# Optimization experiments

Hardware: AMD Instinct MI355X
Metric: run time of the kernel (lower is better)

## Reference

```python
import jax, jax.numpy as jnp
import numpy as np

NUM_HEADS = 8
TOPK = 16


def setup_inputs() -> dict:
    key = jax.random.key(0)
    ks = jax.random.split(key, 13)
    B, C, H, W = 2, 512, 64, 64
    Hu, Wu = H // 2, W // 2
    hd = C // NUM_HEADS
    n = lambda k, shape, s=1.0: jax.random.normal(k, shape, dtype=jnp.float32) * s
    return {
        "x": n(ks[0], (B, C, H, W)),
        "upper_feat": n(ks[1], (B, C, Hu, Wu)),
        "gumbel": jax.random.gumbel(ks[2], (B, NUM_HEADS, Hu * Wu), dtype=jnp.float32),
        # 1x1 convs (Conv2d + folded eval-mode BN => weight matrix + bias)
        "q_w": n(ks[3], (C, C), 0.02), "q_b": n(ks[4], (C,), 0.02),
        "kv_w": n(ks[5], (2 * C, C), 0.02), "kv_b": n(ks[6], (2 * C,), 0.02),
        "proj_w": n(ks[7], (C, C), 0.02), "proj_b": n(ks[8], (C,), 0.02),
        # depthwise 7x7 PE conv (groups = C)
        "pe_w": n(ks[9], (C, 1, 7, 7), 0.02), "pe_b": n(ks[10], (C,), 0.02),
        # gate conv1d kernel_size=1: [head_dim, 2*head_dim]
        "gate_w": n(ks[11], (hd, 2 * hd), 0.02), "gate_b": n(ks[12], (hd,), 0.02),
    }


def reference(x, upper_feat, gumbel, q_w, q_b, kv_w, kv_b, proj_w, proj_b,
              pe_w, pe_b, gate_w, gate_b):
    B, C, H, W = x.shape
    hd = C // NUM_HEADS
    Hu, Wu = upper_feat.shape[2], upper_feat.shape[3]
    N, Nu = H * W, Hu * Wu
    scale = hd ** -0.5

    def conv1x1(t, w, b):
        return jnp.einsum('bchw,oc->bohw', t, w) + b[None, :, None, None]

    # coarse attention: q from x, k/v from upper_feat
    q = conv1x1(x, q_w, q_b).reshape(B, NUM_HEADS, hd, N).transpose(0, 1, 3, 2)          # [B,h,N,d]
    kv = conv1x1(upper_feat, kv_w, kv_b).reshape(B, NUM_HEADS, 2 * hd, Nu).transpose(0, 1, 3, 2)
    k, v = kv[..., :hd], kv[..., hd:]                                                    # [B,h,Nu,d]
    sim = jnp.einsum('bhnd,bhmd->bhnm', q, k) * scale                                    # [B,h,N,Nu]
    attn = jax.nn.softmax(sim, axis=-1)
    coarse = jnp.einsum('bhnm,bhmd->bhnd', attn, v)                                      # [B,h,N,d]

    # fine branch: kv from x, top-k token selection via gumbel-softmax scores
    f_kv = conv1x1(x, kv_w, kv_b).reshape(B, NUM_HEADS, 2 * hd, N).transpose(0, 1, 3, 2)
    f_k, f_v = f_kv[..., :hd], f_kv[..., hd:]                                            # [B,h,N,d]

    # heat: channel-mean of x, adaptive-avg-pooled 2x2 to upper resolution (no grad)
    heat = jax.lax.stop_gradient(
        x.mean(axis=1).reshape(B, Hu, 2, Wu, 2).mean(axis=(2, 4)).reshape(B, Nu))
    global_sim = sim.mean(axis=2) * heat[:, None, :]                                     # [B,h,Nu]
    soft_weights = jax.nn.softmax(global_sim + gumbel, axis=-1)
    _, idx = jax.lax.top_k(soft_weights, TOPK)                                           # [B,h,K]

    # map each selected upper-token to its 2x2 block of x-tokens
    h_idx = (idx // Wu) * 2
    w_idx = (idx % Wu) * 2
    idx_full = jnp.concatenate(
        [(h_idx + dh) * W + (w_idx + dw) for dh in range(2) for dw in range(2)], axis=-1)  # [B,h,4K]

    topk_k = jnp.take_along_axis(f_k, idx_full[..., None], axis=2)                       # [B,h,4K,d]
    topk_v = jnp.take_along_axis(f_v, idx_full[..., None], axis=2)
    fine = jax.nn.softmax(jnp.einsum('bhnd,bhmd->bhnm', q, topk_k) * scale, axis=-1)
    refined = jnp.einsum('bhnm,bhmd->bhnd', fine, topk_v)                                # [B,h,N,d]

    # gated fusion (conv1d kernel_size=1 == per-token linear over 2d channels)
    fusion = jnp.concatenate([coarse, refined], axis=-1)                                 # [B,h,N,2d]
    gate = jax.nn.sigmoid(jnp.einsum('bhnc,oc->bhno', fusion, gate_w) + gate_b)
    out = gate * refined + (1.0 - gate) * coarse                                         # [B,h,N,d]

    x_out = out.transpose(0, 1, 3, 2).reshape(B, C, H, W)

    # positional encoding: depthwise 7x7 conv on v, bilinear upsample to (H,W)
    v_rs = v.transpose(0, 1, 3, 2).reshape(B, C, Hu, Wu)
    v_pe = jax.lax.conv_general_dilated(
        v_rs, pe_w, (1, 1), ((3, 3), (3, 3)), feature_group_count=C,
        dimension_numbers=('NCHW', 'OIHW', 'NCHW')) + pe_b[None, :, None, None]
    v_pe = jax.image.resize(v_pe, (B, C, H, W), method='bilinear')

    return conv1x1(x_out + v_pe, proj_w, proj_b)
```

## Files before the change

kernel.cpp:

```cpp
#include <hip/hip_runtime.h>
#include <hip/hip_bf16.h>
#include <cstdint>

typedef __hip_bfloat16 bf16;
typedef unsigned short u16;
typedef __attribute__((ext_vector_type(8))) short bf16x8;
typedef __attribute__((ext_vector_type(4))) float f32x4;

static __device__ __forceinline__ float b2f(bf16 v) { return __bfloat162float(v); }
static __device__ __forceinline__ float bs2f(u16 s) {
  unsigned int u = ((unsigned int)s) << 16;
  float f;
  __builtin_memcpy(&f, &u, 4);
  return f;
}
static __device__ __forceinline__ u16 f2bs(float f) {
  bf16 h = __float2bfloat16(f);
  u16 s;
  __builtin_memcpy(&s, &h, 2);
  return s;
}
static __device__ __forceinline__ float ldf(const void* p, size_t i, int f32) {
  return f32 ? ((const float*)p)[i] : bs2f(((const u16*)p)[i]);
}

__global__ __launch_bounds__(256) void detect_dtype(const uint4* __restrict__ xs,
                                                    int* __restrict__ flag) {
  int i = blockIdx.x * 256 + threadIdx.x;
  uint4 v = xs[i];
  bool hit = false;
#pragma unroll
  for (int j = 0; j < 4; ++j) {
    unsigned w = (j == 0) ? v.x : (j == 1) ? v.y : (j == 2) ? v.z : v.w;
    if ((w & 0x7F80u) == 0x7F80u) hit = true;
    if ((w & 0x7F800000u) == 0x7F800000u) hit = true;
  }
  unsigned long long mask = __ballot(hit);
  if (mask != 0ull && (threadIdx.x & 63) == 0) atomicOr(flag, 1);
}

__global__ __launch_bounds__(256) void prep_gate(
    const void* __restrict__ gate_w, const void* __restrict__ gate_b,
    u16* __restrict__ gwb, float* __restrict__ gbf,
    const int* __restrict__ dtf) {
  const int f32 = *dtf;
  int t = threadIdx.x;
  for (int i = t; i < 8192; i += 256)
    gwb[i] = f32 ? f2bs(((const float*)gate_w)[i]) : ((const u16*)gate_w)[i];
  if (t < 64) gbf[t] = ldf(gate_b, t, f32);
}

__global__ __launch_bounds__(256) void transpose_bf16(
    const void* __restrict__ src, u16* __restrict__ dst, int N,
    const int* __restrict__ dtf) {
  const int f32 = *dtf;
  const int b = blockIdx.z, n0 = blockIdx.x * 64, c0 = blockIdx.y * 64;
  const int t = threadIdx.x;
  __shared__ __align__(16) u16 tile[64][72];
#pragma unroll
  for (int j = 0; j < 2; ++j) {
    int cc = (t >> 3) + j * 32;
    int nn = (t & 7) * 8;
    u16 tmp[8];
    if (f32) {
      const float* s4 = (const float*)src + ((size_t)(b * 512 + c0 + cc)) * N + n0 + nn;
#pragma unroll
      for (int u = 0; u < 8; ++u) tmp[u] = f2bs(s4[u]);
    } else {
      *reinterpret_cast<uint4*>(tmp) = *reinterpret_cast<const uint4*>(
          (const u16*)src + ((size_t)(b * 512 + c0 + cc)) * N + n0 + nn);
    }
    *reinterpret_cast<uint4*>(&tile[cc][nn]) = *reinterpret_cast<const uint4*>(tmp);
  }
  __syncthreads();
#pragma unroll
  for (int j = 0; j < 2; ++j) {
    int nn = (t >> 3) + j * 32;
    int cc0 = (t & 7) * 8;
    u16 tmp[8];
#pragma unroll
    for (int u = 0; u < 8; ++u) tmp[u] = tile[cc0 + u][nn];
    *reinterpret_cast<uint4*>(&dst[((size_t)b * N + n0 + nn) * 512 + c0 + cc0]) =
        *reinterpret_cast<const uint4*>(tmp);
  }
}

template<int MODE>
__global__ __launch_bounds__(256) void gemm_mfma(
    const u16* __restrict__ A, const void* __restrict__ W,
    const void* __restrict__ bias, u16* __restrict__ o0, u16* __restrict__ o1,
    u16* __restrict__ oT, void* __restrict__ ob, int M,
    const int* __restrict__ dtf) {
  const int f32 = *dtf;
  const int b = blockIdx.z, m0 = blockIdx.x * 64, oo0 = blockIdx.y * 64;
  const int t = threadIdx.x, w = t >> 6, lane = t & 63;
  const int quad = lane >> 4, c = lane & 15;
  __shared__ __align__(16) u16 As[64][72];
  __shared__ __align__(16) u16 Ws[64][72];
  f32x4 acc[4];
#pragma unroll
  for (int ot = 0; ot < 4; ++ot) acc[ot] = (f32x4){0.f, 0.f, 0.f, 0.f};
  const u16* Ab = A + (size_t)b * M * 512;
  const int srow = t >> 2, scol = (t & 3) * 16;

  for (int k0 = 0; k0 < 512; k0 += 64) {
    __syncthreads();
    {
      const u16* ga = Ab + (size_t)(m0 + srow) * 512 + k0 + scol;
      *reinterpret_cast<uint4*>(&As[srow][scol])     = *reinterpret_cast<const uint4*>(ga);
      *reinterpret_cast<uint4*>(&As[srow][scol + 8]) = *reinterpret_cast<const uint4*>(ga + 8);
      if (f32) {
        const float* gw = (const float*)W + (size_t)(oo0 + srow) * 512 + k0 + scol;
#pragma unroll
        for (int e = 0; e < 16; ++e) Ws[srow][scol + e] = f2bs(gw[e]);
      } else {
        const u16* gw = (const u16*)W + (size_t)(oo0 + srow) * 512 + k0 + scol;
        *reinterpret_cast<uint4*>(&Ws[srow][scol])     = *reinterpret_cast<const uint4*>(gw);
        *reinterpret_cast<uint4*>(&Ws[srow][scol + 8]) = *reinterpret_cast<const uint4*>(gw + 8);
      }
    }
    __syncthreads();
#pragma unroll
    for (int ks = 0; ks < 2; ++ks) {
      bf16x8 av = *reinterpret_cast<const bf16x8*>(&As[w * 16 + c][ks * 32 + quad * 8]);
#pragma unroll
      for (int ot = 0; ot < 4; ++ot) {
        bf16x8 wv = *reinterpret_cast<const bf16x8*>(&Ws[ot * 16 + c][ks * 32 + quad * 8]);
        if (MODE == 3)
          acc[ot] = __builtin_amdgcn_mfma_f32_16x16x32_bf16(wv, av, acc[ot], 0, 0, 0);
        else
          acc[ot] = __builtin_amdgcn_mfma_f32_16x16x32_bf16(av, wv, acc[ot], 0, 0, 0);
      }
    }
  }

  if (MODE == 0) {
#pragma unroll
    for (int ot = 0; ot < 4; ++ot) {
      int o = oo0 + ot * 16 + c;
      float bv = ldf(bias, o, f32);
      int h = o >> 6, d = o & 63;
#pragma unroll
      for (int r = 0; r < 4; ++r) {
        int m = m0 + w * 16 + quad * 4 + r;
        o0[((size_t)(b * 8 + h) * M + m) * 64 + d] = f2bs(acc[ot][r] + bv);
      }
    }
  } else if (MODE == 1) {
#pragma unroll
    for (int ot = 0; ot < 4; ++ot) {
      int o = oo0 + ot * 16 + c;
      float bv = ldf(bias, o, f32);
      int hh = o >> 7, jj = o & 127;
#pragma unroll
      for (int r = 0; r < 4; ++r) {
        int m = m0 + w * 16 + quad * 4 + r;
        u16 val = f2bs(acc[ot][r] + bv);
        if (jj < 64) {
          o0[((size_t)(b * 8 + hh) * M + m) * 64 + jj] = val;
        } else {
          o1[((size_t)(b * 8 + hh) * M + m) * 64 + (jj & 63)] = val;
          oT[((size_t)(b * 8 + hh) * 64 + (jj & 63)) * M + m] = val;
        }
      }
    }
  } else {
#pragma unroll
    for (int ot = 0; ot < 4; ++ot) {
#pragma unroll
      for (int r = 0; r < 4; ++r) {
        int o = oo0 + ot * 16 + quad * 4 + r;
        float val = acc[ot][r] + ldf(bias, o, f32);
        int m = m0 + w * 16 + c;
        size_t oi_ = ((size_t)(b * 512 + o)) * M + m;
        if (f32) ((float*)ob)[oi_] = val;
        else     ((u16*)ob)[oi_] = f2bs(val);
      }
    }
  }
}

__global__ __launch_bounds__(256) void heat_kernel(const u16* __restrict__ xT,
                                                   float* __restrict__ heat) {
  int bm = blockIdx.x;
  int b = bm >> 10, mu = bm & 1023;
  int hu = mu >> 5, wu = mu & 31;
  int t = threadIdx.x;
  int row = t >> 6, seg = t & 63;
  int y = hu * 2 + (row >> 1), xx = wu * 2 + (row & 1);
  const uint4* p = reinterpret_cast<const uint4*>(
      xT + ((size_t)b * 4096 + y * 64 + xx) * 512);
  uint4 v = p[seg];
  float s = 0.f;
#pragma unroll
  for (int j = 0; j < 4; ++j) {
    unsigned w = (j == 0) ? v.x : (j == 1) ? v.y : (j == 2) ? v.z : v.w;
    s += bs2f((u16)(w & 0xFFFF)) + bs2f((u16)(w >> 16));
  }
  __shared__ float r[256];
  r[t] = s; __syncthreads();
  for (int off = 128; off; off >>= 1) { if (t < off) r[t] += r[t + off]; __syncthreads(); }
  if (t == 0) heat[bm] = r[0] * (1.0f / 2048.0f);
}

__global__ __launch_bounds__(256) void qsum_partial(const u16* __restrict__ q,
                                                    float* __restrict__ qsumP) {
  int bh = blockIdx.x, ch = blockIdx.y, t = threadIdx.x;
  int d = t & 63, g = t >> 6;
  int n0 = ch * 256 + g * 64;
  float s = 0.f;
  for (int r = 0; r < 64; ++r)
    s += bs2f(q[((size_t)bh * 4096 + n0 + r) * 64 + d]);
  __shared__ float r[256];
  r[t] = s; __syncthreads();
  if (t < 64) qsumP[(size_t)(bh * 16 + ch) * 64 + t] = r[t] + r[t + 64] + r[t + 128] + r[t + 192];
}

__global__ __launch_bounds__(256) void topk_kernel(
    const float* __restrict__ qsumP, const u16* __restrict__ k,
    const float* __restrict__ heat, const void* __restrict__ gumbel,
    int* __restrict__ posb, const int* __restrict__ dtf) {
  const int f32 = *dtf;
  int bh = blockIdx.x, b = bh >> 3, t = threadIdx.x;
  __shared__ float qs[64];
  __shared__ float s[1024];
  __shared__ float rv[256];
  __shared__ int   ri[256];
  if (t < 64) {
    float acc = 0.f;
    for (int ch = 0; ch < 16; ++ch) acc += qsumP[(size_t)(bh * 16 + ch) * 64 + t];
    qs[t] = acc;
  }
  __syncthreads();
  for (int j = 0; j < 4; ++j) {
    int m = t + j * 256;
    const u16* kr = k + ((size_t)bh * 1024 + m) * 64;
    float dot = 0.f;
    for (int d = 0; d < 64; ++d) dot += qs[d] * bs2f(kr[d]);
    s[m] = dot * (0.125f / 4096.0f) * heat[b * 1024 + m] + ldf(gumbel, (size_t)bh * 1024 + m, f32);
  }
  __syncthreads();
  for (int it = 0; it < 16; ++it) {
    float bv = -1e30f; int bi = 0x7fffffff;
    for (int j = 0; j < 4; ++j) {
      int m = t + j * 256; float vv = s[m];
      if (vv > bv || (vv == bv && m < bi)) { bv = vv; bi = m; }
    }
    rv[t] = bv; ri[t] = bi; __syncthreads();
    for (int off = 128; off; off >>= 1) {
      if (t < off) {
        if (rv[t + off] > rv[t] || (rv[t + off] == rv[t] && ri[t + off] < ri[t])) {
          rv[t] = rv[t + off]; ri[t] = ri[t + off];
        }
      }
      __syncthreads();
    }
    if (t == 0) {
      int mi = ri[0]; s[mi] = -1e30f;
      int hy = (mi >> 5) * 2, wx = (mi & 31) * 2;
      posb[bh * 64 + it]      = hy * 64 + wx;
      posb[bh * 64 + 16 + it] = hy * 64 + wx + 1;
      posb[bh * 64 + 32 + it] = (hy + 1) * 64 + wx;
      posb[bh * 64 + 48 + it] = (hy + 1) * 64 + wx + 1;
    }
    __syncthreads();
  }
}

__global__ __launch_bounds__(256) void gather_kv_mfma(
    const u16* __restrict__ xT, const void* __restrict__ kv_w,
    const void* __restrict__ kv_b, const int* __restrict__ posb,
    u16* __restrict__ tkb, u16* __restrict__ tvTb,
    const int* __restrict__ dtf) {
  const int f32 = *dtf;
  const int bh = blockIdx.x, b = bh >> 3, h = bh & 7;
  const int half = blockIdx.y;
  const int t = threadIdx.x, w = t >> 6, lane = t & 63;
  const int quad = lane >> 4, c = lane & 15;
  __shared__ int pos[64];
  __shared__ __align__(16) u16 As[64][72];
  __shared__ __align__(16) u16 Ws[64][72];
  if (t < 64) pos[t] = posb[bh * 64 + t];
  __syncthreads();
  const int obase = h * 128 + half * 64;
  const int srow = t >> 2, scol = (t & 3) * 16;
  const int arow = pos[srow];
  f32x4 acc[4];
#pragma unroll
  for (int ot = 0; ot < 4; ++ot) acc[ot] = (f32x4){0.f, 0.f, 0.f, 0.f};

  for (int k0 = 0; k0 < 512; k0 += 64) {
    __syncthreads();
    {
      const u16* ga = xT + ((size_t)b * 4096 + arow) * 512 + k0 + scol;
      *reinterpret_cast<uint4*>(&As[srow][scol])     = *reinterpret_cast<const uint4*>(ga);
      *reinterpret_cast<uint4*>(&As[srow][scol + 8]) = *reinterpret_cast<const uint4*>(ga + 8);
      if (f32) {
        const float* gw = (const float*)kv_w + (size_t)(obase + srow) * 512 + k0 + scol;
#pragma unroll
        for (int e = 0; e < 16; ++e) Ws[srow][scol + e] = f2bs(gw[e]);
      } else {
        const u16* gw = (const u16*)kv_w + (size_t)(obase + srow) * 512 + k0 + scol;
        *reinterpret_cast<uint4*>(&Ws[srow][scol])     = *reinterpret_cast<const uint4*>(gw);
        *reinterpret_cast<uint4*>(&Ws[srow][scol + 8]) = *reinterpret_cast<const uint4*>(gw + 8);
      }
    }
    __syncthreads();
#pragma unroll
    for (int ks = 0; ks < 2; ++ks) {
      bf16x8 av = *reinterpret_cast<const bf16x8*>(&As[w * 16 + c][ks * 32 + quad * 8]);
#pragma unroll
      for (int ot = 0; ot < 4; ++ot) {
        bf16x8 wv = *reinterpret_cast<const bf16x8*>(&Ws[ot * 16 + c][ks * 32 + quad * 8]);
        acc[ot] = __builtin_amdgcn_mfma_f32_16x16x32_bf16(av, wv, acc[ot], 0, 0, 0);
      }
    }
  }

#pragma unroll
  for (int ot = 0; ot < 4; ++ot) {
    int d = ot * 16 + c;
    float bv = ldf(kv_b, obase + d, f32);
#pragma unroll
    for (int r = 0; r < 4; ++r) {
      int m = w * 16 + quad * 4 + r;
      u16 val = f2bs(acc[ot][r] + bv);
      if (half) tvTb[((size_t)bh * 64 + d) * 64 + m] = val;
      else      tkb[((size_t)bh * 64 + m) * 64 + d] = val;
    }
  }
}

__global__ __launch_bounds__(256) void coarse_attn_mfma(
    const u16* __restrict__ q, const u16* __restrict__ k,
    const u16* __restrict__ vT, u16* __restrict__ coarse) {
  const int bh = blockIdx.y;
  const int n0 = blockIdx.x * 128;
  const int t = threadIdx.x, w = t >> 6, lane = t & 63;
  const int quad = lane >> 4, c = lane & 15;
  __shared__ __align__(16) u16 Ks[2][64][72];
  __shared__ __align__(16) u16 Vt[2][64][72];
  __shared__ __align__(16) u16 Ps[4][2][16][72];

  bf16x8 bq[2][2];
#pragma unroll
  for (int nt = 0; nt < 2; ++nt) {
    const u16* qr = q + ((size_t)bh * 4096 + n0 + w * 32 + nt * 16 + c) * 64;
    bq[nt][0] = *reinterpret_cast<const bf16x8*>(qr + quad * 8);
    bq[nt][1] = *reinterpret_cast<const bf16x8*>(qr + 32 + quad * 8);
  }
  f32x4 po[2][4];
#pragma unroll
  for (int nt = 0; nt < 2; ++nt)
#pragma unroll
    for (int dt = 0; dt < 4; ++dt) po[nt][dt] = (f32x4){0.f, 0.f, 0.f, 0.f};
  float sume[2] = {0.f, 0.f};

  const u16* kbase = k + (size_t)bh * 65536;
  const u16* vbase = vT + (size_t)bh * 65536;
  const int srow = t >> 2, scol = (t & 3) * 16;

  uint4 kr0, kr1, vr0, vr1;
  {
    const u16* gk = kbase + (size_t)srow * 64 + scol;
    kr0 = *reinterpret_cast<const uint4*>(gk);
    kr1 = *reinterpret_cast<const uint4*>(gk + 8);
    const u16* gv = vbase + (size_t)srow * 1024 + scol;
    vr0 = *reinterpret_cast<const uint4*>(gv);
    vr1 = *reinterpret_cast<const uint4*>(gv + 8);
    *reinterpret_cast<uint4*>(&Ks[0][srow][scol])     = kr0;
    *reinterpret_cast<uint4*>(&Ks[0][srow][scol + 8]) = kr1;
    *reinterpret_cast<uint4*>(&Vt[0][srow][scol])     = vr0;
    *reinterpret_cast<uint4*>(&Vt[0][srow][scol + 8]) = vr1;
  }

  for (int ch = 0; ch < 16; ++ch) {
    __syncthreads();
    const int buf = ch & 1;
    if (ch + 1 < 16) {
      int m1 = (ch + 1) * 64;
      const u16* gk = kbase + (size_t)(m1 + srow) * 64 + scol;
      kr0 = *reinterpret_cast<const uint4*>(gk);
      kr1 = *reinterpret_cast<const uint4*>(gk + 8);
      const u16* gv = vbase + (size_t)srow * 1024 + m1 + scol;
      vr0 = *reinterpret_cast<const uint4*>(gv);
      vr1 = *reinterpret_cast<const uint4*>(gv + 8);
    }

    f32x4 st[2][4];
#pragma unroll
    for (int mt = 0; mt < 4; ++mt) {
      bf16x8 ak0 = *reinterpret_cast<const bf16x8*>(&Ks[buf][mt * 16 + c][quad * 8]);
      bf16x8 ak1 = *reinterpret_cast<const bf16x8*>(&Ks[buf][mt * 16 + c][32 + quad * 8]);
#pragma unroll
      for (int nt = 0; nt < 2; ++nt) {
        f32x4 acc = (f32x4){0.f, 0.f, 0.f, 0.f};
        acc = __builtin_amdgcn_mfma_f32_16x16x32_bf16(ak0, bq[nt][0], acc, 0, 0, 0);
        acc = __builtin_amdgcn_mfma_f32_16x16x32_bf16(ak1, bq[nt][1], acc, 0, 0, 0);
        st[nt][mt] = acc;
      }
    }
#pragma unroll
    for (int nt = 0; nt < 2; ++nt) {
      float cs = 0.f;
#pragma unroll
      for (int mt = 0; mt < 4; ++mt) {
        float e0 = __expf(st[nt][mt][0] * 0.125f);
        float e1 = __expf(st[nt][mt][1] * 0.125f);
        float e2 = __expf(st[nt][mt][2] * 0.125f);
        float e3 = __expf(st[nt][mt][3] * 0.125f);
        cs += (e0 + e1) + (e2 + e3);
        ushort4 pw;
        pw.x = f2bs(e0); pw.y = f2bs(e1); pw.z = f2bs(e2); pw.w = f2bs(e3);
        *reinterpret_cast<ushort4*>(&Ps[w][nt][c][mt * 16 + quad * 4]) = pw;
      }
      cs += __shfl_xor(cs, 16, 64);
      cs += __shfl_xor(cs, 32, 64);
      sume[nt] += cs;
    }
#pragma unroll
    for (int s = 0; s < 2; ++s) {
      bf16x8 bp0 = *reinterpret_cast<const bf16x8*>(&Ps[w][0][c][s * 32 + quad * 8]);
      bf16x8 bp1 = *reinterpret_cast<const bf16x8*>(&Ps[w][1][c][s * 32 + quad * 8]);
#pragma unroll
      for (int dt = 0; dt < 4; ++dt) {
        bf16x8 av = *reinterpret_cast<const bf16x8*>(&Vt[buf][dt * 16 + c][s * 32 + quad * 8]);
        po[0][dt] = __builtin_amdgcn_mfma_f32_16x16x32_bf16(av, bp0, po[0][dt], 0, 0, 0);
        po[1][dt] = __builtin_amdgcn_mfma_f32_16x16x32_bf16(av, bp1, po[1][dt], 0, 0, 0);
      }
    }

    if (ch + 1 < 16) {
      const int nb = buf ^ 1;
      *reinterpret_cast<uint4*>(&Ks[nb][srow][scol])     = kr0;
      *reinterpret_cast<uint4*>(&Ks[nb][srow][scol + 8]) = kr1;
      *reinterpret_cast<uint4*>(&Vt[nb][srow][scol])     = vr0;
      *reinterpret_cast<uint4*>(&Vt[nb][srow][scol + 8]) = vr1;
    }
  }

#pragma unroll
  for (int nt = 0; nt < 2; ++nt) {
    float inv = 1.0f / sume[nt];
    u16* orow = coarse + ((size_t)bh * 4096 + n0 + w * 32 + nt * 16 + c) * 64;
#pragma unroll
    for (int dt = 0; dt < 4; ++dt) {
      ushort4 r;
      r.x = f2bs(po[nt][dt][0] * inv); r.y = f2bs(po[nt][dt][1] * inv);
      r.z = f2bs(po[nt][dt][2] * inv); r.w = f2bs(po[nt][dt][3] * inv);
      *reinterpret_cast<ushort4*>(&orow[dt * 16 + quad * 4]) = r;
    }
  }
}

__global__ __launch_bounds__(256) void dwconv_kernel(
    const u16* __restrict__ v, const void* __restrict__ pe_w,
    const void* __restrict__ pe_b, u16* __restrict__ vpe,
    const int* __restrict__ dtf) {
  const int f32 = *dtf;
  int bc = blockIdx.x;
  int b = bc >> 9, c = bc & 511;
  int h = c >> 6, d = c & 63;
  int t = threadIdx.x;
  __shared__ float img[1024];
  __shared__ float wts[49];
  for (int i = t; i < 1024; i += 256)
    img[i] = bs2f(v[((size_t)(b * 8 + h) * 1024 + i) * 64 + d]);
  if (t < 49) wts[t] = ldf(pe_w, c * 49 + t, f32);
  float bias = ldf(pe_b, c, f32);
  __syncthreads();
  for (int i = t; i < 1024; i += 256) {
    int y = i >> 5, xx = i & 31;
    float a = 0.f;
#pragma unroll
    for (int ky = 0; ky < 7; ++ky) {
      int yy = y + ky - 3;
      if ((unsigned)yy >= 32u) continue;
#pragma unroll
      for (int kx = 0; kx < 7; ++kx) {
        int xc = xx + kx - 3;
        if ((unsigned)xc >= 32u) continue;
        a += img[yy * 32 + xc] * wts[ky * 7 + kx];
      }
    }
    vpe[(size_t)bc * 1024 + i] = f2bs(a + bias);
  }
}

__global__ __launch_bounds__(256) void fine_mfma(
    const u16* __restrict__ q, const u16* __restrict__ tkb,
    const u16* __restrict__ tvTb, const u16* __restrict__ co,
    const u16* __restrict__ gwb, const float* __restrict__ gbf,
    const u16* __restrict__ vpe, u16* __restrict__ xsT) {
  const int bh = blockIdx.y, b = bh >> 3, h = bh & 7;
  const int y = blockIdx.x;
  const int n0 = y * 64;
  const int t = threadIdx.x, w = t >> 6, lane = t & 63;
  const int quad = lane >> 4, c = lane & 15;

  __shared__ __align__(16) u16 fus[4][16][136];
  __shared__ __align__(16) u16 vl[2][64][40];
  __shared__ float gbl[64];

  int jy = y >> 1, y0, y1; float wy0, wy1;
  if ((y & 1) == 0) { y0 = (jy > 0) ? jy - 1 : 0; y1 = jy; wy0 = 0.25f; wy1 = 0.75f; }
  else              { y0 = jy; y1 = (jy < 31) ? jy + 1 : 31; wy0 = 0.75f; wy1 = 0.25f; }

  for (int idx = t; idx < 512; idx += 256) {
    int seg = idx & 3, ch = (idx >> 2) & 63, r = idx >> 8;
    int yy = r ? y1 : y0;
    const uint4* src = reinterpret_cast<const uint4*>(
        vpe + ((size_t)(b * 512 + h * 64 + ch)) * 1024 + yy * 32);
    *reinterpret_cast<uint4*>(&vl[r][ch][seg * 8]) = src[seg];
  }
  if (t < 64) gbl[t] = gbf[t];

  const int n = n0 + w * 16 + c;
  bf16x8 bq[2];
  {
    const u16* qr = q + ((size_t)bh * 4096 + n) * 64;
    bq[0] = *reinterpret_cast<const bf16x8*>(qr + quad * 8);
    bq[1] = *reinterpret_cast<const bf16x8*>(qr + 32 + quad * 8);
  }
  __syncthreads();

  f32x4 st[4];
#pragma unroll
  for (int mt = 0; mt < 4; ++mt) {
    f32x4 acc = (f32x4){0.f, 0.f, 0.f, 0.f};
#pragma unroll
    for (int s = 0; s < 2; ++s) {
      bf16x8 ak = *reinterpret_cast<const bf16x8*>(
          &tkb[((size_t)bh * 64 + mt * 16 + c) * 64 + s * 32 + quad * 8]);
      acc = __builtin_amdgcn_mfma_f32_16x16x32_bf16(ak, bq[s], acc, 0, 0, 0);
    }
    st[mt] = acc;
  }
  float sume = 0.f;
#pragma unroll
  for (int mt = 0; mt < 4; ++mt) {
    float e0 = __expf(st[mt][0] * 0.125f);
    float e1 = __expf(st[mt][1] * 0.125f);
    float e2 = __expf(st[mt][2] * 0.125f);
    float e3 = __expf(st[mt][3] * 0.125f);
    sume += (e0 + e1) + (e2 + e3);
    ushort4 pw;
    pw.x = f2bs(e0); pw.y = f2bs(e1); pw.z = f2bs(e2); pw.w = f2bs(e3);
    *reinterpret_cast<ushort4*>(&fus[w][c][mt * 16 + quad * 4]) = pw;
  }
  sume += __shfl_xor(sume, 16, 64);
  sume += __shfl_xor(sume, 32, 64);
  float inv = 1.0f / sume;

  f32x4 po[4];
#pragma unroll
  for (int dt = 0; dt < 4; ++dt) po[dt] = (f32x4){0.f, 0.f, 0.f, 0.f};
#pragma unroll
  for (int s = 0; s < 2; ++s) {
    bf16x8 bp = *reinterpret_cast<const bf16x8*>(&fus[w][c][s * 32 + quad * 8]);
#pragma unroll
    for (int dt = 0; dt < 4; ++dt) {
      bf16x8 av = *reinterpret_cast<const bf16x8*>(
          &tvTb[((size_t)bh * 64 + dt * 16 + c) * 64 + s * 32 + quad * 8]);
      po[dt] = __builtin_amdgcn_mfma_f32_16x16x32_bf16(av, bp, po[dt], 0, 0, 0);
    }
  }

  {
    const u16* crow = co + ((size_t)bh * 4096 + n) * 64 + quad * 16;
    *reinterpret_cast<uint4*>(&fus[w][c][quad * 16])     = *reinterpret_cast<const uint4*>(crow);
    *reinterpret_cast<uint4*>(&fus[w][c][quad * 16 + 8]) = *reinterpret_cast<const uint4*>(crow + 8);
  }
#pragma unroll
  for (int dt = 0; dt < 4; ++dt) {
    ushort4 rw;
    rw.x = f2bs(po[dt][0] * inv); rw.y = f2bs(po[dt][1] * inv);
    rw.z = f2bs(po[dt][2] * inv); rw.w = f2bs(po[dt][3] * inv);
    *reinterpret_cast<ushort4*>(&fus[w][c][64 + dt * 16 + quad * 4]) = rw;
  }

  f32x4 ga[4];
#pragma unroll
  for (int ot = 0; ot < 4; ++ot) ga[ot] = (f32x4){0.f, 0.f, 0.f, 0.f};
#pragma unroll
  for (int s = 0; s < 4; ++s) {
    bf16x8 bf = *reinterpret_cast<const bf16x8*>(&fus[w][c][s * 32 + quad * 8]);
#pragma unroll
    for (int ot = 0; ot < 4; ++ot) {
      bf16x8 ag = *reinterpret_cast<const bf16x8*>(
          gwb + (ot * 16 + c) * 128 + s * 32 + quad * 8);
      ga[ot] = __builtin_amdgcn_mfma_f32_16x16x32_bf16(ag, bf, ga[ot], 0, 0, 0);
    }
  }

  const int x = w * 16 + c;
  int jx = x >> 1, x0, x1; float wx0, wx1;
  if ((x & 1) == 0) { x0 = (jx > 0) ? jx - 1 : 0; x1 = jx; wx0 = 0.25f; wx1 = 0.75f; }
  else              { x0 = jx; x1 = (jx < 31) ? jx + 1 : 31; wx0 = 0.75f; wx1 = 0.25f; }
#pragma unroll
  for (int dt = 0; dt < 4; ++dt) {
    ushort4 ow;
    u16 tmp[4];
#pragma unroll
    for (int r = 0; r < 4; ++r) {
      int row = dt * 16 + quad * 4 + r;
      float ref = po[dt][r] * inv;
      float coar = bs2f(fus[w][c][row]);
      float g = 1.0f / (1.0f + __expf(-(ga[dt][r] + gbl[row])));
      float vv = wy0 * (wx0 * bs2f(vl[0][row][x0]) + wx1 * bs2f(vl[0][row][x1])) +
                 wy1 * (wx0 * bs2f(vl[1][row][x0]) + wx1 * bs2f(vl[1][row][x1]));
      tmp[r] = f2bs(g * ref + (1.0f - g) * coar + vv);
    }
    ow.x = tmp[0]; ow.y = tmp[1]; ow.z = tmp[2]; ow.w = tmp[3];
    *reinterpret_cast<ushort4*>(&fus[w][c][dt * 16 + quad * 4]) = ow;
  }

  {
    int nl = lane >> 2, cs = (lane & 3) * 16;
    u16* dst = xsT + ((size_t)b * 4096 + n0 + w * 16 + nl) * 512 + h * 64 + cs;
    *reinterpret_cast<uint4*>(dst)     = *reinterpret_cast<const uint4*>(&fus[w][nl][cs]);
    *reinterpret_cast<uint4*>(dst + 8) = *reinterpret_cast<const uint4*>(&fus[w][nl][cs + 8]);
  }
}

extern "C" void kernel_launch(void* const* d_in, const int* in_sizes, int n_in,
                              void* d_out, int out_size, void* d_ws, size_t ws_size,
                              hipStream_t stream) {
  const void* x    = d_in[0];
  const void* up   = d_in[1];
  const void* gum  = d_in[2];
  const void* q_w  = d_in[3];
  const void* q_b  = d_in[4];
  const void* kv_w = d_in[5];
  const void* kv_b = d_in[6];
  const void* p_w  = d_in[7];
  const void* p_b  = d_in[8];
  const void* pe_w = d_in[9];
  const void* pe_b = d_in[10];
  const void* g_w  = d_in[11];
  const void* g_b  = d_in[12];

  float* ws    = (float*)d_ws;
  int*   dtf   = (int*)ws;
  float* qsumP = ws + 16;
  float* heat  = qsumP + 16384;
  int*   posb  = (int*)(heat + 2048);
  float* gbf   = (float*)(posb + 1024);
  u16*   gwb   = (u16*)(gbf + 64);
  u16*   tkb   = gwb + 8192;
  u16*   tvTb  = tkb + 65536;
  u16*   qb    = tvTb + 65536;
  u16*   kb    = qb + 4194304;
  u16*   vb    = kb + 1048576;
  u16*   vTb   = vb + 1048576;
  u16*   xT    = vTb + 1048576;
  u16*   upT   = xT + 4194304;
  u16*   co    = upT + 1048576;
  u16*   xsT   = co + 4194304;
  u16*   vpe   = xsT + 4194304;

  dim3 blk(256);
  hipMemsetAsync(dtf, 0, 4, stream);
  detect_dtype<<<dim3(64), blk, 0, stream>>>((const uint4*)x, dtf);
  prep_gate<<<dim3(1), blk, 0, stream>>>(g_w, g_b, gwb, gbf, dtf);
  transpose_bf16<<<dim3(64, 8, 2), blk, 0, stream>>>(x, xT, 4096, dtf);
  transpose_bf16<<<dim3(16, 8, 2), blk, 0, stream>>>(up, upT, 1024, dtf);
  heat_kernel<<<dim3(2048), blk, 0, stream>>>(xT, heat);
  gemm_mfma<0><<<dim3(64, 8, 2), blk, 0, stream>>>(xT, q_w, q_b, qb, nullptr, nullptr, nullptr, 4096, dtf);
  gemm_mfma<1><<<dim3(16, 16, 2), blk, 0, stream>>>(upT, kv_w, kv_b, kb, vb, vTb, nullptr, 1024, dtf);
  qsum_partial<<<dim3(16, 16), blk, 0, stream>>>(qb, qsumP);
  topk_kernel<<<dim3(16), blk, 0, stream>>>(qsumP, kb, heat, gum, posb, dtf);
  gather_kv_mfma<<<dim3(16, 2), blk, 0, stream>>>(xT, kv_w, kv_b, posb, tkb, tvTb, dtf);
  coarse_attn_mfma<<<dim3(32, 16), blk, 0, stream>>>(qb, kb, vTb, co);
  dwconv_kernel<<<dim3(1024), blk, 0, stream>>>(vb, pe_w, pe_b, vpe, dtf);
  fine_mfma<<<dim3(64, 16), blk, 0, stream>>>(qb, tkb, tvTb, co, gwb, gbf, vpe, xsT);
  gemm_mfma<3><<<dim3(64, 8, 2), blk, 0, stream>>>(xsT, p_w, p_b, nullptr, nullptr, nullptr, d_out, 4096, dtf);
}
```

Baseline: 279.3 us.

## Fuse heat and q-sum reductions into producers, enlarge GEMM tiles, drop v copy

```diff
diff --git a/kernel.cpp b/kernel.cpp
--- a/kernel.cpp
+++ b/kernel.cpp
@@ -7,7 +7,6 @@
 typedef __attribute__((ext_vector_type(8))) short bf16x8;
 typedef __attribute__((ext_vector_type(4))) float f32x4;
 
-static __device__ __forceinline__ float b2f(bf16 v) { return __bfloat162float(v); }
 static __device__ __forceinline__ float bs2f(u16 s) {
   unsigned int u = ((unsigned int)s) << 16;
   float f;
@@ -52,7 +51,7 @@
 
 __global__ __launch_bounds__(256) void transpose_bf16(
     const void* __restrict__ src, u16* __restrict__ dst, int N,
-    const int* __restrict__ dtf) {
+    float* __restrict__ heat, const int* __restrict__ dtf) {
   const int f32 = *dtf;
   const int b = blockIdx.z, n0 = blockIdx.x * 64, c0 = blockIdx.y * 64;
   const int t = threadIdx.x;
@@ -73,6 +72,14 @@
     *reinterpret_cast<uint4*>(&tile[cc][nn]) = *reinterpret_cast<const uint4*>(tmp);
   }
   __syncthreads();
+  if (heat != nullptr && t < 32) {
+    float s = 0.f;
+#pragma unroll 8
+    for (int cc = 0; cc < 64; ++cc)
+      s += bs2f(tile[cc][2 * t]) + bs2f(tile[cc][2 * t + 1]);
+    int y = blockIdx.x;
+    atomicAdd(&heat[b * 1024 + (y >> 1) * 32 + t], s);
+  }
 #pragma unroll
   for (int j = 0; j < 2; ++j) {
     int nn = (t >> 3) + j * 32;
@@ -86,11 +93,107 @@
 }
 
 template<int MODE>
-__global__ __launch_bounds__(256) void gemm_mfma(
+__global__ __launch_bounds__(256) void gemm128(
     const u16* __restrict__ A, const void* __restrict__ W,
-    const void* __restrict__ bias, u16* __restrict__ o0, u16* __restrict__ o1,
-    u16* __restrict__ oT, void* __restrict__ ob, int M,
+    const void* __restrict__ bias, u16* __restrict__ o0,
+    void* __restrict__ ob, float* __restrict__ qsum, int M,
     const int* __restrict__ dtf) {
+  const int f32 = *dtf;
+  const int b = blockIdx.z, m0 = blockIdx.x * 128, oo0 = blockIdx.y * 64;
+  const int t = threadIdx.x, w = t >> 6, lane = t & 63;
+  const int quad = lane >> 4, c = lane & 15;
+  __shared__ __align__(16) u16 As[128][72];
+  __shared__ __align__(16) u16 Ws[64][72];
+  f32x4 acc[2][4];
+#pragma unroll
+  for (int nt = 0; nt < 2; ++nt)
+#pragma unroll
+    for (int ot = 0; ot < 4; ++ot) acc[nt][ot] = (f32x4){0.f, 0.f, 0.f, 0.f};
+  const u16* Ab = A + (size_t)b * M * 512;
+  const int arow = t >> 1, acol = (t & 1) * 32;
+  const int wrow = t >> 2, wcol = (t & 3) * 16;
+
+  for (int k0 = 0; k0 < 512; k0 += 64) {
+    __syncthreads();
+    {
+      const u16* ga = Ab + (size_t)(m0 + arow) * 512 + k0 + acol;
+      uint4* ad = reinterpret_cast<uint4*>(&As[arow][acol]);
+      const uint4* gs = reinterpret_cast<const uint4*>(ga);
+      ad[0] = gs[0]; ad[1] = gs[1]; ad[2] = gs[2]; ad[3] = gs[3];
+      if (f32) {
+        const float* gw = (const float*)W + (size_t)(oo0 + wrow) * 512 + k0 + wcol;
+#pragma unroll
+        for (int e = 0; e < 16; ++e) Ws[wrow][wcol + e] = f2bs(gw[e]);
+      } else {
+        const u16* gw = (const u16*)W + (size_t)(oo0 + wrow) * 512 + k0 + wcol;
+        *reinterpret_cast<uint4*>(&Ws[wrow][wcol])     = *reinterpret_cast<const uint4*>(gw);
+        *reinterpret_cast<uint4*>(&Ws[wrow][wcol + 8]) = *reinterpret_cast<const uint4*>(gw + 8);
+      }
+    }
+    __syncthreads();
+#pragma unroll
+    for (int ks = 0; ks < 2; ++ks) {
+      bf16x8 av[2];
+      av[0] = *reinterpret_cast<const bf16x8*>(&As[w * 32 + c][ks * 32 + quad * 8]);
+      av[1] = *reinterpret_cast<const bf16x8*>(&As[w * 32 + 16 + c][ks * 32 + quad * 8]);
+#pragma unroll
+      for (int ot = 0; ot < 4; ++ot) {
+        bf16x8 wv = *reinterpret_cast<const bf16x8*>(&Ws[ot * 16 + c][ks * 32 + quad * 8]);
+#pragma unroll
+        for (int nt = 0; nt < 2; ++nt) {
+          if (MODE == 3)
+            acc[nt][ot] = __builtin_amdgcn_mfma_f32_16x16x32_bf16(wv, av[nt], acc[nt][ot], 0, 0, 0);
+          else
+            acc[nt][ot] = __builtin_amdgcn_mfma_f32_16x16x32_bf16(av[nt], wv, acc[nt][ot], 0, 0, 0);
+        }
+      }
+    }
+  }
+
+  if (MODE == 0) {
+    const int h = oo0 >> 6, bh = b * 8 + h;
+#pragma unroll
+    for (int ot = 0; ot < 4; ++ot) {
+      int o = oo0 + ot * 16 + c;
+      int d = o & 63;
+      float bv = ldf(bias, o, f32);
+      float qs = 0.f;
+#pragma unroll
+      for (int nt = 0; nt < 2; ++nt)
+#pragma unroll
+        for (int r = 0; r < 4; ++r) {
+          int m = m0 + w * 32 + nt * 16 + quad * 4 + r;
+          u16 val = f2bs(acc[nt][ot][r] + bv);
+          o0[((size_t)bh * M + m) * 64 + d] = val;
+          qs += bs2f(val);
+        }
+      qs += __shfl_xor(qs, 16, 64);
+      qs += __shfl_xor(qs, 32, 64);
+      if (quad == 0) atomicAdd(&qsum[bh * 64 + d], qs);
+    }
+  } else {
+#pragma unroll
+    for (int ot = 0; ot < 4; ++ot)
+#pragma unroll
+      for (int r = 0; r < 4; ++r) {
+        int o = oo0 + ot * 16 + quad * 4 + r;
+        float bv = ldf(bias, o, f32);
+#pragma unroll
+        for (int nt = 0; nt < 2; ++nt) {
+          int m = m0 + w * 32 + nt * 16 + c;
+          float val = acc[nt][ot][r] + bv;
+          size_t oi_ = ((size_t)(b * 512 + o)) * M + m;
+          if (f32) ((float*)ob)[oi_] = val;
+          else     ((u16*)ob)[oi_] = f2bs(val);
+        }
+      }
+  }
+}
+
+__global__ __launch_bounds__(256) void gemm_kv(
+    const u16* __restrict__ A, const void* __restrict__ W,
+    const void* __restrict__ bias, u16* __restrict__ kb, u16* __restrict__ vTb,
+    int M, const int* __restrict__ dtf) {
   const int f32 = *dtf;
   const int b = blockIdx.z, m0 = blockIdx.x * 64, oo0 = blockIdx.y * 64;
   const int t = threadIdx.x, w = t >> 6, lane = t & 63;
@@ -126,98 +229,28 @@
 #pragma unroll
       for (int ot = 0; ot < 4; ++ot) {
         bf16x8 wv = *reinterpret_cast<const bf16x8*>(&Ws[ot * 16 + c][ks * 32 + quad * 8]);
-        if (MODE == 3)
-          acc[ot] = __builtin_amdgcn_mfma_f32_16x16x32_bf16(wv, av, acc[ot], 0, 0, 0);
-        else
-          acc[ot] = __builtin_amdgcn_mfma_f32_16x16x32_bf16(av, wv, acc[ot], 0, 0, 0);
-      }
-    }
-  }
-
-  if (MODE == 0) {
-#pragma unroll
-    for (int ot = 0; ot < 4; ++ot) {
-      int o = oo0 + ot * 16 + c;
-      float bv = ldf(bias, o, f32);
-      int h = o >> 6, d = o & 63;
-#pragma unroll
-      for (int r = 0; r < 4; ++r) {
-        int m = m0 + w * 16 + quad * 4 + r;
-        o0[((size_t)(b * 8 + h) * M + m) * 64 + d] = f2bs(acc[ot][r] + bv);
-      }
-    }
-  } else if (MODE == 1) {
-#pragma unroll
-    for (int ot = 0; ot < 4; ++ot) {
-      int o = oo0 + ot * 16 + c;
-      float bv = ldf(bias, o, f32);
-      int hh = o >> 7, jj = o & 127;
-#pragma unroll
-      for (int r = 0; r < 4; ++r) {
-        int m = m0 + w * 16 + quad * 4 + r;
-        u16 val = f2bs(acc[ot][r] + bv);
-        if (jj < 64) {
-          o0[((size_t)(b * 8 + hh) * M + m) * 64 + jj] = val;
-        } else {
-          o1[((size_t)(b * 8 + hh) * M + m) * 64 + (jj & 63)] = val;
-          oT[((size_t)(b * 8 + hh) * 64 + (jj & 63)) * M + m] = val;
-        }
-      }
-    }
-  } else {
-#pragma unroll
-    for (int ot = 0; ot < 4; ++ot) {
-#pragma unroll
-      for (int r = 0; r < 4; ++r) {
-        int o = oo0 + ot * 16 + quad * 4 + r;
-        float val = acc[ot][r] + ldf(bias, o, f32);
-        int m = m0 + w * 16 + c;
-        size_t oi_ = ((size_t)(b * 512 + o)) * M + m;
-        if (f32) ((float*)ob)[oi_] = val;
-        else     ((u16*)ob)[oi_] = f2bs(val);
-      }
-    }
-  }
-}
-
-__global__ __launch_bounds__(256) void heat_kernel(const u16* __restrict__ xT,
-                                                   float* __restrict__ heat) {
-  int bm = blockIdx.x;
-  int b = bm >> 10, mu = bm & 1023;
-  int hu = mu >> 5, wu = mu & 31;
-  int t = threadIdx.x;
-  int row = t >> 6, seg = t & 63;
-  int y = hu * 2 + (row >> 1), xx = wu * 2 + (row & 1);
-  const uint4* p = reinterpret_cast<const uint4*>(
-      xT + ((size_t)b * 4096 + y * 64 + xx) * 512);
-  uint4 v = p[seg];
-  float s = 0.f;
-#pragma unroll
-  for (int j = 0; j < 4; ++j) {
-    unsigned w = (j == 0) ? v.x : (j == 1) ? v.y : (j == 2) ? v.z : v.w;
-    s += bs2f((u16)(w & 0xFFFF)) + bs2f((u16)(w >> 16));
-  }
-  __shared__ float r[256];
-  r[t] = s; __syncthreads();
-  for (int off = 128; off; off >>= 1) { if (t < off) r[t] += r[t + off]; __syncthreads(); }
-  if (t == 0) heat[bm] = r[0] * (1.0f / 2048.0f);
-}
-
-__global__ __launch_bounds__(256) void qsum_partial(const u16* __restrict__ q,
-                                                    float* __restrict__ qsumP) {
-  int bh = blockIdx.x, ch = blockIdx.y, t = threadIdx.x;
-  int d = t & 63, g = t >> 6;
-  int n0 = ch * 256 + g * 64;
-  float s = 0.f;
-  for (int r = 0; r < 64; ++r)
-    s += bs2f(q[((size_t)bh * 4096 + n0 + r) * 64 + d]);
-  __shared__ float r[256];
-  r[t] = s; __syncthreads();
-  if (t < 64) qsumP[(size_t)(bh * 16 + ch) * 64 + t] = r[t] + r[t + 64] + r[t + 128] + r[t + 192];
+        acc[ot] = __builtin_amdgcn_mfma_f32_16x16x32_bf16(av, wv, acc[ot], 0, 0, 0);
+      }
+    }
+  }
+
+#pragma unroll
+  for (int ot = 0; ot < 4; ++ot) {
+    int o = oo0 + ot * 16 + c;
+    float bv = ldf(bias, o, f32);
+    int hh = o >> 7, jj = o & 127;
+#pragma unroll
+    for (int r = 0; r < 4; ++r) {
+      int m = m0 + w * 16 + quad * 4 + r;
+      u16 val = f2bs(acc[ot][r] + bv);
+      if (jj < 64) kb[((size_t)(b * 8 + hh) * M + m) * 64 + jj] = val;
+      else         vTb[((size_t)(b * 8 + hh) * 64 + (jj & 63)) * M + m] = val;
+    }
+  }
 }
 
 __global__ __launch_bounds__(256) void topk_kernel(
-    const float* __restrict__ qsumP, const u16* __restrict__ k,
+    const float* __restrict__ qsum, const u16* __restrict__ k,
     const float* __restrict__ heat, const void* __restrict__ gumbel,
     int* __restrict__ posb, const int* __restrict__ dtf) {
   const int f32 = *dtf;
@@ -226,18 +259,15 @@
   __shared__ float s[1024];
   __shared__ float rv[256];
   __shared__ int   ri[256];
-  if (t < 64) {
-    float acc = 0.f;
-    for (int ch = 0; ch < 16; ++ch) acc += qsumP[(size_t)(bh * 16 + ch) * 64 + t];
-    qs[t] = acc;
-  }
+  if (t < 64) qs[t] = qsum[bh * 64 + t];
   __syncthreads();
   for (int j = 0; j < 4; ++j) {
     int m = t + j * 256;
     const u16* kr = k + ((size_t)bh * 1024 + m) * 64;
     float dot = 0.f;
     for (int d = 0; d < 64; ++d) dot += qs[d] * bs2f(kr[d]);
-    s[m] = dot * (0.125f / 4096.0f) * heat[b * 1024 + m] + ldf(gumbel, (size_t)bh * 1024 + m, f32);
+    s[m] = dot * (0.125f / 4096.0f) * (heat[b * 1024 + m] * (1.0f / 2048.0f)) +
+           ldf(gumbel, (size_t)bh * 1024 + m, f32);
   }
   __syncthreads();
   for (int it = 0; it < 16; ++it) {
@@ -454,7 +484,7 @@
 }
 
 __global__ __launch_bounds__(256) void dwconv_kernel(
-    const u16* __restrict__ v, const void* __restrict__ pe_w,
+    const u16* __restrict__ vT, const void* __restrict__ pe_w,
     const void* __restrict__ pe_b, u16* __restrict__ vpe,
     const int* __restrict__ dtf) {
   const int f32 = *dtf;
@@ -464,8 +494,14 @@
   int t = threadIdx.x;
   __shared__ float img[1024];
   __shared__ float wts[49];
-  for (int i = t; i < 1024; i += 256)
-    img[i] = bs2f(v[((size_t)(b * 8 + h) * 1024 + i) * 64 + d]);
+  const u16* base = vT + ((size_t)(b * 8 + h) * 64 + d) * 1024;
+  if (t < 128) {
+    uint4 v4 = reinterpret_cast<const uint4*>(base)[t];
+    u16 tmp[8];
+    *reinterpret_cast<uint4*>(tmp) = v4;
+#pragma unroll
+    for (int e = 0; e < 8; ++e) img[t * 8 + e] = bs2f(tmp[e]);
+  }
   if (t < 49) wts[t] = ldf(pe_w, c * 49 + t, f32);
   float bias = ldf(pe_b, c, f32);
   __syncthreads();
@@ -642,8 +678,8 @@
 
   float* ws    = (float*)d_ws;
   int*   dtf   = (int*)ws;
-  float* qsumP = ws + 16;
-  float* heat  = qsumP + 16384;
+  float* qsum  = ws + 16;
+  float* heat  = qsum + 1024;
   int*   posb  = (int*)(heat + 2048);
   float* gbf   = (float*)(posb + 1024);
   u16*   gwb   = (u16*)(gbf + 64);
@@ -651,8 +687,7 @@
   u16*   tvTb  = tkb + 65536;
   u16*   qb    = tvTb + 65536;
   u16*   kb    = qb + 4194304;
-  u16*   vb    = kb + 1048576;
-  u16*   vTb   = vb + 1048576;
+  u16*   vTb   = kb + 1048576;
   u16*   xT    = vTb + 1048576;
   u16*   upT   = xT + 4194304;
   u16*   co    = upT + 1048576;
@@ -660,19 +695,17 @@
   u16*   vpe   = xsT + 4194304;
 
   dim3 blk(256);
-  hipMemsetAsync(dtf, 0, 4, stream);
+  hipMemsetAsync(ws, 0, (16 + 1024 + 2048) * 4, stream);
   detect_dtype<<<dim3(64), blk, 0, stream>>>((const uint4*)x, dtf);
   prep_gate<<<dim3(1), blk, 0, stream>>>(g_w, g_b, gwb, gbf, dtf);
-  transpose_bf16<<<dim3(64, 8, 2), blk, 0, stream>>>(x, xT, 4096, dtf);
-  transpose_bf16<<<dim3(16, 8, 2), blk, 0, stream>>>(up, upT, 1024, dtf);
-  heat_kernel<<<dim3(2048), blk, 0, stream>>>(xT, heat);
-  gemm_mfma<0><<<dim3(64, 8, 2), blk, 0, stream>>>(xT, q_w, q_b, qb, nullptr, nullptr, nullptr, 4096, dtf);
-  gemm_mfma<1><<<dim3(16, 16, 2), blk, 0, stream>>>(upT, kv_w, kv_b, kb, vb, vTb, nullptr, 1024, dtf);
-  qsum_partial<<<dim3(16, 16), blk, 0, stream>>>(qb, qsumP);
-  topk_kernel<<<dim3(16), blk, 0, stream>>>(qsumP, kb, heat, gum, posb, dtf);
+  transpose_bf16<<<dim3(64, 8, 2), blk, 0, stream>>>(x, xT, 4096, heat, dtf);
+  transpose_bf16<<<dim3(16, 8, 2), blk, 0, stream>>>(up, upT, 1024, nullptr, dtf);
+  gemm128<0><<<dim3(32, 8, 2), blk, 0, stream>>>(xT, q_w, q_b, qb, nullptr, qsum, 4096, dtf);
+  gemm_kv<<<dim3(16, 16, 2), blk, 0, stream>>>(upT, kv_w, kv_b, kb, vTb, 1024, dtf);
+  topk_kernel<<<dim3(16), blk, 0, stream>>>(qsum, kb, heat, gum, posb, dtf);
   gather_kv_mfma<<<dim3(16, 2), blk, 0, stream>>>(xT, kv_w, kv_b, posb, tkb, tvTb, dtf);
   coarse_attn_mfma<<<dim3(32, 16), blk, 0, stream>>>(qb, kb, vTb, co);
-  dwconv_kernel<<<dim3(1024), blk, 0, stream>>>(vb, pe_w, pe_b, vpe, dtf);
+  dwconv_kernel<<<dim3(1024), blk, 0, stream>>>(vTb, pe_w, pe_b, vpe, dtf);
   fine_mfma<<<dim3(64, 16), blk, 0, stream>>>(qb, tkb, tvTb, co, gwb, gbf, vpe, xsT);
-  gemm_mfma<3><<<dim3(64, 8, 2), blk, 0, stream>>>(xsT, p_w, p_b, nullptr, nullptr, nullptr, d_out, 4096, dtf);
-}
+  gemm128<3><<<dim3(32, 8, 2), blk, 0, stream>>>(xsT, p_w, p_b, nullptr, d_out, nullptr, 4096, dtf);
+}
```

After: 271.7 us. 1.03x faster.
